# Optimization experiments

Measured on AMD Instinct MI355X. Metric: run time of the kernel, lower is better.

The kernel has to match this reference:

```python
import jax, jax.numpy as jnp
import numpy as np

N = 120000
GRID = (480, 360, 32)
C_IN, C0, C1 = 16, 32, 64
EPS = 1e-5


def _build_rulebook(coords, lut, offsets, grid, n):
    # coords: [N,3] active voxel coords; lut: dense linear-index -> row (n = inactive)
    g = np.array(grid)
    cols = []
    for off in offsets:
        nc = coords + np.array(off)
        valid = np.all((nc >= 0) & (nc < g), axis=1)
        ncl = np.clip(nc, 0, g - 1)
        nlin = np.ravel_multi_index((ncl[:, 0], ncl[:, 1], ncl[:, 2]), grid)
        cols.append(np.where(valid, lut[nlin], n))
    return np.stack(cols, axis=1).astype(np.int32)  # [N, 9]


def setup_inputs() -> dict:
    rng = np.random.default_rng(0)
    total = GRID[0] * GRID[1] * GRID[2]
    lin = rng.choice(total, N, replace=False)
    coords = np.stack(np.unravel_index(lin, GRID), axis=1)
    lut = np.full(total, N, dtype=np.int32)
    lut[lin] = np.arange(N, dtype=np.int32)
    offs133 = [(0, dy, dz) for dy in (-1, 0, 1) for dz in (-1, 0, 1)]  # kernel (1,3,3)
    offs313 = [(dx, 0, dz) for dx in (-1, 0, 1) for dz in (-1, 0, 1)]  # kernel (3,1,3)
    nbr133 = jnp.asarray(_build_rulebook(coords, lut, offs133, GRID, N))
    nbr313 = jnp.asarray(_build_rulebook(coords, lut, offs313, GRID, N))

    key = jax.random.key(0)
    ks = jax.random.split(key, 9)

    def w(k, ci, co):
        return jax.random.normal(k, (9, ci, co), jnp.float32) * (1.0 / np.sqrt(9 * ci))

    ones = lambda c: jnp.ones((c,), jnp.float32)
    zeros = lambda c: jnp.zeros((c,), jnp.float32)
    return dict(
        x=jax.random.normal(ks[0], (N, C_IN), jnp.float32),
        nbr133=nbr133, nbr313=nbr313,
        W_c1=w(ks[1], C_IN, C0), g0=ones(C0), b0=zeros(C0),
        W_c12=w(ks[2], C0, C0), g02=ones(C0), b02=zeros(C0),
        W_c2=w(ks[3], C_IN, C0),
        W_c3=w(ks[4], C0, C0), g2=ones(C0), b2=zeros(C0),
        W_r1=w(ks[5], C0, C1), rg0=ones(C1), rb0=zeros(C1),
        W_r12=w(ks[6], C1, C1), rg02=ones(C1), rb02=zeros(C1),
        W_r2=w(ks[7], C0, C1), rg1=ones(C1), rb1=zeros(C1),
        W_r3=w(ks[8], C1, C1), rg2=ones(C1), rb2=zeros(C1),
    )


def _subm(x, nbr, W):
    # submanifold conv as rulebook gather-GEMM: pad row N with zeros for missing neighbors
    xp = jnp.concatenate([x, jnp.zeros((1, x.shape[1]), x.dtype)], axis=0)
    return jnp.einsum('nkc,kcd->nd', xp[nbr], W)  # [N, Cout]


def _bn(x, g, b):
    # BatchNorm1d over active voxels (training-mode batch stats, biased var)
    m = x.mean(axis=0)
    v = x.var(axis=0)
    return (x - m) / jnp.sqrt(v + EPS) * g + b


_lrelu = jax.nn.leaky_relu  # slope 0.01 = torch default


def reference(x, nbr133, nbr313, W_c1, g0, b0, W_c12, g02, b02, W_c2, W_c3, g2, b2,
              W_r1, rg0, rb0, W_r12, rg02, rb02, W_r2, rg1, rb1, W_r3, rg2, rb2):
    # ResContextBlock(16->32): conv -> act -> bn chains
    s = _bn(_lrelu(_subm(x, nbr133, W_c1)), g0, b0)
    s = _bn(_lrelu(_subm(s, nbr313, W_c12)), g02, b02)
    r = _lrelu(_subm(x, nbr313, W_c2))  # bn1 result discarded in source (reaA typo) -> faithfully skipped
    r = _bn(_lrelu(_subm(r, nbr133, W_c3)), g2, b2)
    y = r + s
    # ResBlock(32->64, pooling=False)
    s2 = _bn(_lrelu(_subm(y, nbr313, W_r1)), rg0, rb0)
    s2 = _bn(_lrelu(_subm(s2, nbr133, W_r12)), rg02, rb02)
    r2 = _bn(_lrelu(_subm(y, nbr133, W_r2)), rg1, rb1)
    r2 = _bn(_lrelu(_subm(r2, nbr313, W_r3)), rg2, rb2)
    return r2 + s2  # [N, 64]
```

## Files before the change

### kernel.cpp

```cpp
#include <hip/hip_runtime.h>
#include <hip/hip_bf16.h>

#define N_VOX 120000
#define NTILES (N_VOX / 16)

typedef __attribute__((ext_vector_type(8))) __bf16 bf16x8;
typedef __attribute__((ext_vector_type(4))) float floatx4;
using bf16 = __hip_bfloat16;

__device__ __forceinline__ float b2f(bf16 v) { return __bfloat162float(v); }
__device__ __forceinline__ bf16 f2b(float v) { return __float2bfloat16(v); }

__device__ __forceinline__ bf16x8 gload16(const bf16* p) {
    bf16x8 r;
    asm volatile("global_load_dwordx4 %0, %1, off" : "=v"(r) : "v"(p));
    return r;
}
__device__ __forceinline__ int gloadi(const int* p) {
    int r;
    asm volatile("global_load_dword %0, %1, off" : "=v"(r) : "v"(p));
    return r;
}
__device__ __forceinline__ void gstore16(bf16* p, bf16x8 v) {
    asm volatile("global_store_dwordx4 %0, %1, off" :: "v"(p), "v"(v) : "memory");
}
__device__ __forceinline__ void vm_wait0() { asm volatile("s_waitcnt vmcnt(0)" ::: "memory"); }
__device__ __forceinline__ void vm_wait1() { asm volatile("s_waitcnt vmcnt(1)" ::: "memory"); }
__device__ __forceinline__ void vm_wait2() { asm volatile("s_waitcnt vmcnt(2)" ::: "memory"); }
__device__ __forceinline__ void vm_wait3() { asm volatile("s_waitcnt vmcnt(3)" ::: "memory"); }
__device__ __forceinline__ void pin(bf16x8& x) { asm volatile("" : "+v"(x)); }
__device__ __forceinline__ void pini(int& x)   { asm volatile("" : "+v"(x)); }

template<int CIN, int COUT, int NW, bool STATS>
__global__ __launch_bounds__(NW * 64) void conv_kernel(
    const bf16* __restrict__ uin,
    const int*  __restrict__ nbr,
    const bf16* __restrict__ bpack,
    bf16* __restrict__ tout,
    float* __restrict__ stats)
{
    constexpr int NT = COUT / 16;
    constexpr int K = 9 * CIN;
    constexpr int KSTEPS = (K + 31) / 32;
    constexpr bool BLDS = (COUT == 64);
    constexpr int NFRAG = KSTEPS * NT;
    constexpr int NSTORE = (16 * COUT) / 512;

    __shared__ bf16x8 Bs[BLDS ? NFRAG * 64 : 1];
    __shared__ int idxb[NW][2][192];
    __shared__ __align__(16) bf16 tbuf[NW][16 * COUT];
    __shared__ float sS[64], sS2[64];

    const int lane = threadIdx.x & 63;
    const int wave = threadIdx.x >> 6;
    const int m    = lane & 15;
    const int quad = lane >> 4;

    if (STATS && threadIdx.x < 64) { sS[threadIdx.x] = 0.f; sS2[threadIdx.x] = 0.f; }

    const bf16x8* bp = reinterpret_cast<const bf16x8*>(bpack);
    bf16x8 Bf[BLDS ? 1 : NFRAG];
    if constexpr (BLDS) {
        for (int f = threadIdx.x; f < NFRAG * 64; f += NW * 64) Bs[f] = bp[f];
    } else {
#pragma unroll
        for (int f = 0; f < NFRAG; ++f) Bf[f] = bp[f * 64 + lane];
    }
    __syncthreads();

    float ssum[NT], ssum2[NT];
#pragma unroll
    for (int c = 0; c < NT; ++c) { ssum[c] = 0.f; ssum2[c] = 0.f; }

    const int STRIDE = gridDim.x * NW;
    const int t0 = blockIdx.x * NW + wave;

    {
        const int* b0 = nbr + t0 * 144;
        int i0 = gloadi(b0 + lane);
        int i1 = gloadi(b0 + 64 + lane);
        int i2 = gloadi(b0 + 128 + (lane & 15));
        vm_wait0();
        pini(i0); pini(i1); pini(i2);
        int* ib = idxb[wave][0];
        ib[lane] = i0; ib[64 + lane] = i1; ib[128 + (lane & 15)] = i2;
    }

    int p = 0;
    for (int tile = t0; tile < NTILES; tile += STRIDE) {
        const int* ib = idxb[wave][p];
        int idx[9];
#pragma unroll
        for (int nb = 0; nb < 9; ++nb) idx[nb] = ib[m * 9 + nb];

        bf16x8 a[KSTEPS];
#pragma unroll
        for (int t = 0; t < KSTEPS; ++t) {
            const bf16* src;
            if constexpr (CIN == 64) {
                src = uin + (((size_t)idx[t >> 1]) << 6) + ((t & 1) << 5) + quad * 8;
            } else if constexpr (CIN == 32) {
                src = uin + (((size_t)idx[t]) << 5) + quad * 8;
            } else {
                constexpr int KS = 9 * 16;
                const int j1 = (2 * t + 1 > 8) ? 8 : 2 * t + 1;
                int r_ = (quad & 2) ? idx[j1] : idx[2 * t];
                if (t * 32 + 24 >= KS) {
                    if (t * 32 + quad * 8 >= KS) r_ = N_VOX;
                }
                src = uin + (((size_t)r_) << 4) + ((quad & 1) << 3);
            }
            a[t] = gload16(src);
        }

        const int tnext = (tile + STRIDE < NTILES) ? tile + STRIDE : tile;
        const int* bn_ = nbr + tnext * 144;
        int i0 = gloadi(bn_ + lane);
        int i1 = gloadi(bn_ + 64 + lane);
        int i2 = gloadi(bn_ + 128 + (lane & 15));

        vm_wait3();
#pragma unroll
        for (int t = 0; t < KSTEPS; ++t) pin(a[t]);

        floatx4 acc[NT];
#pragma unroll
        for (int c = 0; c < NT; ++c) acc[c] = (floatx4){0.f, 0.f, 0.f, 0.f};
#pragma unroll
        for (int t = 0; t < KSTEPS; ++t) {
#pragma unroll
            for (int c = 0; c < NT; ++c) {
                const bf16x8 b = BLDS ? Bs[(t * NT + c) * 64 + lane] : Bf[t * NT + c];
                acc[c] = __builtin_amdgcn_mfma_f32_16x16x32_bf16(a[t], b, acc[c], 0, 0, 0);
            }
        }

        bf16* tb = tbuf[wave];
#pragma unroll
        for (int c = 0; c < NT; ++c) {
            float ps = 0.f, ps2 = 0.f;
#pragma unroll
            for (int i = 0; i < 4; ++i) {
                float v = acc[c][i];
                v = v > 0.f ? v : 0.01f * v;
                tb[(quad * 4 + i) * COUT + c * 16 + m] = f2b(v);
                ps += v; ps2 += v * v;
            }
            ssum[c] += ps; ssum2[c] += ps2;
        }
#pragma unroll
        for (int g = 0; g < NSTORE; ++g) {
            const int off = g * 512 + lane * 8;
            bf16x8 row = *reinterpret_cast<const bf16x8*>(tb + off);
            gstore16(tout + (size_t)tile * (16 * COUT) + off, row);
        }

        if constexpr (NSTORE == 2) vm_wait2(); else vm_wait1();
        pini(i0); pini(i1); pini(i2);
        int* ibn = idxb[wave][p ^ 1];
        ibn[lane] = i0; ibn[64 + lane] = i1; ibn[128 + (lane & 15)] = i2;
        p ^= 1;
    }

    if constexpr (STATS) {
#pragma unroll
        for (int c = 0; c < NT; ++c) {
            atomicAdd(&sS[c * 16 + m], ssum[c]);
            atomicAdd(&sS2[c * 16 + m], ssum2[c]);
        }
        __syncthreads();
        if (threadIdx.x < COUT) {
            atomicAdd(&stats[threadIdx.x],      sS[threadIdx.x]);
            atomicAdd(&stats[64 + threadIdx.x], sS2[threadIdx.x]);
        }
    }
}

template<int C>
__global__ __launch_bounds__(256) void bnapply_kernel(
    bf16* t, const float* __restrict__ s,
    const float* __restrict__ g, const float* __restrict__ b)
{
    __shared__ float pa[64], pc[64];
    if (threadIdx.x < C) {
        const float inv_n = 1.0f / N_VOX;
        const float mu = s[threadIdx.x] * inv_n;
        const float var = fmaxf(s[64 + threadIdx.x] * inv_n - mu * mu, 0.f);
        const float a = rsqrtf(var + 1e-5f) * g[threadIdx.x];
        pa[threadIdx.x] = a;
        pc[threadIdx.x] = b[threadIdx.x] - mu * a;
    }
    __syncthreads();
    const int i8 = (blockIdx.x * 256 + threadIdx.x) * 8;
    if (i8 >= (N_VOX + 1) * C) return;
    if (i8 >= N_VOX * C) {
        uint4 z = {0, 0, 0, 0};
        *reinterpret_cast<uint4*>(t + i8) = z;
        return;
    }
    union { bf16x8 v; bf16 e[8]; } U, O;
    U.v = *reinterpret_cast<const bf16x8*>(t + i8);
    const int ch0 = i8 & (C - 1);
#pragma unroll
    for (int j = 0; j < 8; ++j)
        O.e[j] = f2b(pa[ch0 + j] * b2f(U.e[j]) + pc[ch0 + j]);
    *reinterpret_cast<bf16x8*>(t + i8) = O.v;
}

template<int C, bool ZROW, typename OUT>
__global__ __launch_bounds__(256) void addbn_kernel(
    const bf16* ta, const float* __restrict__ sa,
    const float* __restrict__ ga, const float* __restrict__ ba,
    const bf16* tb, const float* __restrict__ sb,
    const float* __restrict__ gb, const float* __restrict__ bb,
    OUT* out)
{
    __shared__ float paa[64], pca[64], pab[64], pcb[64];
    if (threadIdx.x < C) {
        const float inv_n = 1.0f / N_VOX;
        const float ma = sa[threadIdx.x] * inv_n;
        const float va = fmaxf(sa[64 + threadIdx.x] * inv_n - ma * ma, 0.f);
        const float aa = rsqrtf(va + 1e-5f) * ga[threadIdx.x];
        paa[threadIdx.x] = aa;
        pca[threadIdx.x] = ba[threadIdx.x] - ma * aa;
        const float mb = sb[threadIdx.x] * inv_n;
        const float vb = fmaxf(sb[64 + threadIdx.x] * inv_n - mb * mb, 0.f);
        const float ab = rsqrtf(vb + 1e-5f) * gb[threadIdx.x];
        pab[threadIdx.x] = ab;
        pcb[threadIdx.x] = bb[threadIdx.x] - mb * ab;
    }
    __syncthreads();
    constexpr int TOTAL = (N_VOX + (ZROW ? 1 : 0)) * C;
    const int i8 = (blockIdx.x * 256 + threadIdx.x) * 8;
    if (i8 >= TOTAL) return;
    if (ZROW && i8 >= N_VOX * C) {
        uint4 z = {0, 0, 0, 0};
        *reinterpret_cast<uint4*>((bf16*)out + i8) = z;
        return;
    }
    union { bf16x8 v; bf16 e[8]; } A, B;
    A.v = *reinterpret_cast<const bf16x8*>(ta + i8);
    B.v = *reinterpret_cast<const bf16x8*>(tb + i8);
    const int ch0 = i8 & (C - 1);
    float r[8];
#pragma unroll
    for (int j = 0; j < 8; ++j)
        r[j] = paa[ch0 + j] * b2f(A.e[j]) + pca[ch0 + j]
             + pab[ch0 + j] * b2f(B.e[j]) + pcb[ch0 + j];
    if constexpr (sizeof(OUT) == 2) {
        union { bf16x8 v; bf16 e[8]; } O;
#pragma unroll
        for (int j = 0; j < 8; ++j) O.e[j] = f2b(r[j]);
        *reinterpret_cast<bf16x8*>(out + i8) = O.v;
    } else {
#pragma unroll
        for (int j = 0; j < 8; ++j) out[i8 + j] = r[j];
    }
}

#define PACK_TOTAL 139264
__global__ __launch_bounds__(256) void prep_kernel(
    const float* __restrict__ x,
    const float* W0, const float* W1, const float* W2, const float* W3,
    const float* W4, const float* W5, const float* W6, const float* W7,
    bf16* __restrict__ u0, bf16* __restrict__ bpack,
    float* __restrict__ stats, bf16* __restrict__ u3)
{
    const int gid = blockIdx.x * 256 + threadIdx.x;
    constexpr int NXE = (N_VOX + 1) * 16;
    if (gid < NXE) {
        u0[gid] = (gid < N_VOX * 16) ? f2b(x[gid]) : f2b(0.f);
        return;
    }
    int p = gid - NXE;
    if (p < PACK_TOTAL) {
        constexpr int cin[8]  = {16, 32, 16, 32, 32, 64, 32, 64};
        constexpr int cout[8] = {32, 32, 32, 32, 64, 64, 64, 64};
        constexpr int offs[9] = {0, 5120, 14336, 19456, 28672, 47104, 83968, 102400, 139264};
        const float* Ws[8] = {W0, W1, W2, W3, W4, W5, W6, W7};
        int w = 0;
        while (p >= offs[w + 1]) ++w;
        const int e = p - offs[w];
        const int CI = cin[w], CO = cout[w];
        const int NTl = CO / 16;
        const int j = e & 7;
        const int lane = (e >> 3) & 63;
        const int rest = e >> 9;
        const int c = rest % NTl;
        const int t = rest / NTl;
        const int ncol = c * 16 + (lane & 15);
        const int k = t * 32 + (lane >> 4) * 8 + j;
        float val = 0.f;
        if (k < 9 * CI) {
            const int nbq = k / CI;
            const int ci = k % CI;
            val = Ws[w][(nbq * CI + ci) * CO + ncol];
        }
        bpack[p] = f2b(val);
        return;
    }
    p -= PACK_TOTAL;
    if (p < 1024) { stats[p] = 0.f; return; }
    p -= 1024;
    if (p < 32) u3[N_VOX * 32 + p] = f2b(0.f);
}

extern "C" void kernel_launch(void* const* d_in, const int* in_sizes, int n_in,
                              void* d_out, int out_size, void* d_ws, size_t ws_size,
                              hipStream_t stream) {
    const float* x     = (const float*)d_in[0];
    const int* nbr133  = (const int*)d_in[1];
    const int* nbr313  = (const int*)d_in[2];
    const float* W_c1  = (const float*)d_in[3];
    const float* g0    = (const float*)d_in[4];
    const float* b0    = (const float*)d_in[5];
    const float* W_c12 = (const float*)d_in[6];
    const float* g02   = (const float*)d_in[7];
    const float* b02   = (const float*)d_in[8];
    const float* W_c2  = (const float*)d_in[9];
    const float* W_c3  = (const float*)d_in[10];
    const float* g2    = (const float*)d_in[11];
    const float* b2    = (const float*)d_in[12];
    const float* W_r1  = (const float*)d_in[13];
    const float* rg0   = (const float*)d_in[14];
    const float* rb0   = (const float*)d_in[15];
    const float* W_r12 = (const float*)d_in[16];
    const float* rg02  = (const float*)d_in[17];
    const float* rb02  = (const float*)d_in[18];
    const float* W_r2  = (const float*)d_in[19];
    const float* rg1   = (const float*)d_in[20];
    const float* rb1   = (const float*)d_in[21];
    const float* W_r3  = (const float*)d_in[22];
    const float* rg2   = (const float*)d_in[23];
    const float* rb2   = (const float*)d_in[24];

    char* ws = (char*)d_ws;
    size_t off = 0;
    auto alloc = [&](size_t bytes) -> char* {
        off = (off + 255) & ~(size_t)255;
        char* p = ws + off;
        off += bytes;
        return p;
    };
    const size_t NV = N_VOX;
    bf16* u0   = (bf16*)alloc((NV + 1) * 16 * 2);
    bf16* B1u3 = (bf16*)alloc((NV + 1) * 32 * 2);
    bf16* T4   = (bf16*)alloc(NV * 32 * 2);
    bf16* T2uy = (bf16*)alloc((NV + 1) * 32 * 2);
    bf16* B5B7 = (bf16*)alloc((NV + 1) * 64 * 2);
    bf16* T8   = (bf16*)alloc(NV * 64 * 2);
    bf16* bpack = (bf16*)alloc((size_t)PACK_TOTAL * 2);
    float* stats = (float*)alloc(1024 * 4);
    bf16* T6 = (bf16*)ws;

    float* st1 = stats + 0 * 128;
    float* st2 = stats + 1 * 128;
    float* st4 = stats + 3 * 128;
    float* st5 = stats + 4 * 128;
    float* st6 = stats + 5 * 128;
    float* st7 = stats + 6 * 128;
    float* st8 = stats + 7 * 128;

    bf16* bp0 = bpack + 0;
    bf16* bp1 = bpack + 5120;
    bf16* bp2 = bpack + 14336;
    bf16* bp3 = bpack + 19456;
    bf16* bp4 = bpack + 28672;
    bf16* bp5 = bpack + 47104;
    bf16* bp6 = bpack + 83968;
    bf16* bp7 = bpack + 102400;

    const int prep_total = (N_VOX + 1) * 16 + PACK_TOTAL + 1024 + 32;
    prep_kernel<<<(prep_total + 255) / 256, 256, 0, stream>>>(
        x, W_c1, W_c12, W_c2, W_c3, W_r1, W_r12, W_r2, W_r3, u0, bpack, stats, B1u3);

    const int E32 = (((N_VOX + 1) * 32) / 8 + 255) / 256;
    const int E64 = (((N_VOX + 1) * 64) / 8 + 255) / 256;

    conv_kernel<16, 32, 4, true><<<768, 256, 0, stream>>>(u0, nbr133, bp0, B1u3, st1);
    bnapply_kernel<32><<<E32, 256, 0, stream>>>(B1u3, st1, g0, b0);
    conv_kernel<32, 32, 4, true><<<768, 256, 0, stream>>>(B1u3, nbr313, bp1, T2uy, st2);
    conv_kernel<16, 32, 4, false><<<768, 256, 0, stream>>>(u0, nbr313, bp2, B1u3, nullptr);
    conv_kernel<32, 32, 4, true><<<768, 256, 0, stream>>>(B1u3, nbr133, bp3, T4, st4);
    addbn_kernel<32, true, bf16><<<E32, 256, 0, stream>>>(
        T2uy, st2, g02, b02, T4, st4, g2, b2, T2uy);
    conv_kernel<32, 64, 8, true><<<512, 512, 0, stream>>>(T2uy, nbr313, bp4, B5B7, st5);
    bnapply_kernel<64><<<E64, 256, 0, stream>>>(B5B7, st5, rg0, rb0);
    conv_kernel<64, 64, 16, true><<<256, 1024, 0, stream>>>(B5B7, nbr133, bp5, T6, st6);
    conv_kernel<32, 64, 8, true><<<512, 512, 0, stream>>>(T2uy, nbr133, bp6, B5B7, st7);
    bnapply_kernel<64><<<E64, 256, 0, stream>>>(B5B7, st7, rg1, rb1);
    conv_kernel<64, 64, 16, true><<<256, 1024, 0, stream>>>(B5B7, nbr313, bp7, T8, st8);
    addbn_kernel<64, false, float><<<((N_VOX * 64 / 8) + 255) / 256, 256, 0, stream>>>(
        T6, st6, rg02, rb02, T8, st8, rg2, rb2, (float*)d_out);
}
```

Measured before the change: 323.7 us.

## Batch independent sparse conv branches into paired launches

Independent convolution branches (conv1/conv3, conv2/conv4-chain, r1/r2, and their BN applies) are merged into single launches that dispatch blocks to one of two problem descriptors by block index. This doubles the per-launch work and cuts kernel launches and tail idle time between dependent small kernels. Buffers are reassigned to avoid aliasing, and the 64-channel convs switch from 16 to 8 waves per block. It relies on scratch buffers being large enough for the new padding-row writes.

```diff
diff --git a/kernel.cpp b/kernel.cpp
--- a/kernel.cpp
+++ b/kernel.cpp
@@ -31,13 +31,11 @@
 __device__ __forceinline__ void pin(bf16x8& x) { asm volatile("" : "+v"(x)); }
 __device__ __forceinline__ void pini(int& x)   { asm volatile("" : "+v"(x)); }
 
-template<int CIN, int COUT, int NW, bool STATS>
-__global__ __launch_bounds__(NW * 64) void conv_kernel(
-    const bf16* __restrict__ uin,
-    const int*  __restrict__ nbr,
-    const bf16* __restrict__ bpack,
-    bf16* __restrict__ tout,
-    float* __restrict__ stats)
+template<int CIN, int COUT, int NW>
+__device__ __forceinline__ void conv_body(
+    const bf16* __restrict__ uin, const int* __restrict__ nbr,
+    const bf16* __restrict__ bpack, bf16* __restrict__ tout,
+    float* __restrict__ stats, int bid, int nblk)
 {
     constexpr int NT = COUT / 16;
     constexpr int K = 9 * CIN;
@@ -56,7 +54,7 @@
     const int m    = lane & 15;
     const int quad = lane >> 4;
 
-    if (STATS && threadIdx.x < 64) { sS[threadIdx.x] = 0.f; sS2[threadIdx.x] = 0.f; }
+    if (threadIdx.x < 64) { sS[threadIdx.x] = 0.f; sS2[threadIdx.x] = 0.f; }
 
     const bf16x8* bp = reinterpret_cast<const bf16x8*>(bpack);
     bf16x8 Bf[BLDS ? 1 : NFRAG];
@@ -72,8 +70,8 @@
 #pragma unroll
     for (int c = 0; c < NT; ++c) { ssum[c] = 0.f; ssum2[c] = 0.f; }
 
-    const int STRIDE = gridDim.x * NW;
-    const int t0 = blockIdx.x * NW + wave;
+    const int STRIDE = nblk * NW;
+    const int t0 = bid * NW + wave;
 
     {
         const int* b0 = nbr + t0 * 144;
@@ -162,7 +160,7 @@
         p ^= 1;
     }
 
-    if constexpr (STATS) {
+    if (stats != nullptr) {
 #pragma unroll
         for (int c = 0; c < NT; ++c) {
             atomicAdd(&sS[c * 16 + m], ssum[c]);
@@ -176,10 +174,35 @@
     }
 }
 
+template<int CIN, int COUT, int NW>
+__global__ __launch_bounds__(NW * 64) void conv_kernel(
+    const bf16* __restrict__ uin, const int* __restrict__ nbr,
+    const bf16* __restrict__ bpack, bf16* __restrict__ tout,
+    float* __restrict__ stats)
+{
+    conv_body<CIN, COUT, NW>(uin, nbr, bpack, tout, stats, blockIdx.x, gridDim.x);
+}
+
+template<int CIN, int COUT, int NW>
+__global__ __launch_bounds__(NW * 64) void conv2_kernel(
+    int GA,
+    const bf16* uinA, const int* nbrA, const bf16* bpA, bf16* toutA, float* stA,
+    const bf16* uinB, const int* nbrB, const bf16* bpB, bf16* toutB, float* stB)
+{
+    const bool isB = (int)blockIdx.x >= GA;
+    const int bid = isB ? (int)blockIdx.x - GA : (int)blockIdx.x;
+    const bf16* uin   = isB ? uinB : uinA;
+    const int*  nbr   = isB ? nbrB : nbrA;
+    const bf16* bpack = isB ? bpB  : bpA;
+    bf16*       tout  = isB ? toutB : toutA;
+    float*      stats = isB ? stB  : stA;
+    conv_body<CIN, COUT, NW>(uin, nbr, bpack, tout, stats, bid, GA);
+}
+
 template<int C>
-__global__ __launch_bounds__(256) void bnapply_kernel(
+__device__ __forceinline__ void bnapply_body(
     bf16* t, const float* __restrict__ s,
-    const float* __restrict__ g, const float* __restrict__ b)
+    const float* __restrict__ g, const float* __restrict__ b, int bid)
 {
     __shared__ float pa[64], pc[64];
     if (threadIdx.x < C) {
@@ -191,7 +214,7 @@
         pc[threadIdx.x] = b[threadIdx.x] - mu * a;
     }
     __syncthreads();
-    const int i8 = (blockIdx.x * 256 + threadIdx.x) * 8;
+    const int i8 = (bid * 256 + threadIdx.x) * 8;
     if (i8 >= (N_VOX + 1) * C) return;
     if (i8 >= N_VOX * C) {
         uint4 z = {0, 0, 0, 0};
@@ -205,6 +228,24 @@
     for (int j = 0; j < 8; ++j)
         O.e[j] = f2b(pa[ch0 + j] * b2f(U.e[j]) + pc[ch0 + j]);
     *reinterpret_cast<bf16x8*>(t + i8) = O.v;
+}
+
+template<int C>
+__global__ __launch_bounds__(256) void bnapply_kernel(
+    bf16* t, const float* __restrict__ s,
+    const float* __restrict__ g, const float* __restrict__ b)
+{
+    bnapply_body<C>(t, s, g, b, blockIdx.x);
+}
+
+__global__ __launch_bounds__(256) void bnapply2_kernel(
+    int GA, bf16* tA, const float* sA, const float* gA, const float* bA,
+    bf16* tB, const float* sB, const float* gB, const float* bB)
+{
+    const bool isB = (int)blockIdx.x >= GA;
+    const int bid = isB ? (int)blockIdx.x - GA : (int)blockIdx.x;
+    bnapply_body<64>(isB ? tB : tA, isB ? sB : sA, isB ? gB : gA,
+                     isB ? bB : bA, bid);
 }
 
 template<int C, bool ZROW, typename OUT>
@@ -264,7 +305,7 @@
     const float* W0, const float* W1, const float* W2, const float* W3,
     const float* W4, const float* W5, const float* W6, const float* W7,
     bf16* __restrict__ u0, bf16* __restrict__ bpack,
-    float* __restrict__ stats, bf16* __restrict__ u3)
+    float* __restrict__ stats, bf16* __restrict__ u3, bf16* __restrict__ u3b)
 {
     const int gid = blockIdx.x * 256 + threadIdx.x;
     constexpr int NXE = (N_VOX + 1) * 16;
@@ -302,7 +343,9 @@
     p -= PACK_TOTAL;
     if (p < 1024) { stats[p] = 0.f; return; }
     p -= 1024;
-    if (p < 32) u3[N_VOX * 32 + p] = f2b(0.f);
+    if (p < 32) { u3[N_VOX * 32 + p] = f2b(0.f); return; }
+    p -= 32;
+    if (p < 32) u3b[N_VOX * 32 + p] = f2b(0.f);
 }
 
 extern "C" void kernel_launch(void* const* d_in, const int* in_sizes, int n_in,
@@ -370,26 +413,27 @@
     bf16* bp6 = bpack + 83968;
     bf16* bp7 = bpack + 102400;
 
-    const int prep_total = (N_VOX + 1) * 16 + PACK_TOTAL + 1024 + 32;
+    const int prep_total = (N_VOX + 1) * 16 + PACK_TOTAL + 1024 + 32 + 32;
     prep_kernel<<<(prep_total + 255) / 256, 256, 0, stream>>>(
-        x, W_c1, W_c12, W_c2, W_c3, W_r1, W_r12, W_r2, W_r3, u0, bpack, stats, B1u3);
+        x, W_c1, W_c12, W_c2, W_c3, W_r1, W_r12, W_r2, W_r3,
+        u0, bpack, stats, B1u3, T2uy);
 
     const int E32 = (((N_VOX + 1) * 32) / 8 + 255) / 256;
     const int E64 = (((N_VOX + 1) * 64) / 8 + 255) / 256;
 
-    conv_kernel<16, 32, 4, true><<<768, 256, 0, stream>>>(u0, nbr133, bp0, B1u3, st1);
+    conv2_kernel<16, 32, 4><<<1536, 256, 0, stream>>>(
+        768, u0, nbr133, bp0, B1u3, st1, u0, nbr313, bp2, T2uy, nullptr);
     bnapply_kernel<32><<<E32, 256, 0, stream>>>(B1u3, st1, g0, b0);
-    conv_kernel<32, 32, 4, true><<<768, 256, 0, stream>>>(B1u3, nbr313, bp1, T2uy, st2);
-    conv_kernel<16, 32, 4, false><<<768, 256, 0, stream>>>(u0, nbr313, bp2, B1u3, nullptr);
-    conv_kernel<32, 32, 4, true><<<768, 256, 0, stream>>>(B1u3, nbr133, bp3, T4, st4);
+    conv2_kernel<32, 32, 4><<<1536, 256, 0, stream>>>(
+        768, B1u3, nbr313, bp1, T4, st2, T2uy, nbr133, bp3, B5B7, st4);
     addbn_kernel<32, true, bf16><<<E32, 256, 0, stream>>>(
-        T2uy, st2, g02, b02, T4, st4, g2, b2, T2uy);
-    conv_kernel<32, 64, 8, true><<<512, 512, 0, stream>>>(T2uy, nbr313, bp4, B5B7, st5);
-    bnapply_kernel<64><<<E64, 256, 0, stream>>>(B5B7, st5, rg0, rb0);
-    conv_kernel<64, 64, 16, true><<<256, 1024, 0, stream>>>(B5B7, nbr133, bp5, T6, st6);
-    conv_kernel<32, 64, 8, true><<<512, 512, 0, stream>>>(T2uy, nbr133, bp6, B5B7, st7);
-    bnapply_kernel<64><<<E64, 256, 0, stream>>>(B5B7, st7, rg1, rb1);
-    conv_kernel<64, 64, 16, true><<<256, 1024, 0, stream>>>(B5B7, nbr313, bp7, T8, st8);
+        T4, st2, g02, b02, B5B7, st4, g2, b2, T2uy);
+    conv2_kernel<32, 64, 8><<<1024, 512, 0, stream>>>(
+        512, T2uy, nbr313, bp4, B5B7, st5, T2uy, nbr133, bp6, T8, st7);
+    bnapply2_kernel<<<2 * E64, 256, 0, stream>>>(
+        E64, B5B7, st5, rg0, rb0, T8, st7, rg1, rb1);
+    conv_kernel<64, 64, 8><<<256, 512, 0, stream>>>(B5B7, nbr133, bp5, T6, st6);
+    conv_kernel<64, 64, 8><<<256, 512, 0, stream>>>(T8, nbr313, bp7, B5B7, st8);
     addbn_kernel<64, false, float><<<((N_VOX * 64 / 8) + 255) / 256, 256, 0, stream>>>(
-        T6, st6, rg02, rb02, T8, st8, rg2, rb2, (float*)d_out);
-}
+        T6, st6, rg02, rb02, B5B7, st8, rg2, rb2, (float*)d_out);
+}
```

New measurement: 293.8 us. 1.1x faster.
